# Kernel tuning notes

Measured on AMD Instinct MI355X. Metric: run time of the kernel, lower is better.

Reference implementation:

```python
import jax, jax.numpy as jnp
import numpy as np

B, N, D, H = 16, 729, 1152, 16
HD = D // H


def setup_inputs() -> dict:
    key = jax.random.key(0)
    ks = jax.random.split(key, 11)
    s = 0.02
    hidden_states = jax.random.normal(ks[0], (B, N, D), dtype=jnp.float32)
    # ToMe token sizes: positive merge counts in [1, 9)
    size = 1.0 + 8.0 * jax.random.uniform(ks[1], (B, N, 1), dtype=jnp.float32)
    Wq = s * jax.random.normal(ks[2], (D, D), dtype=jnp.float32)
    bq = jnp.zeros((D,), jnp.float32)
    Wk = s * jax.random.normal(ks[3], (D, D), dtype=jnp.float32)
    bk = jnp.zeros((D,), jnp.float32)
    Wv = s * jax.random.normal(ks[4], (D, D), dtype=jnp.float32)
    bv = jnp.zeros((D,), jnp.float32)
    Wo = s * jax.random.normal(ks[5], (D, D), dtype=jnp.float32)
    bo = jnp.zeros((D,), jnp.float32)
    return {"hidden_states": hidden_states, "size": size,
            "Wq": Wq, "bq": bq, "Wk": Wk, "bk": bk,
            "Wv": Wv, "bv": bv, "Wo": Wo, "bo": bo}


def reference(hidden_states, size, Wq, bq, Wk, bk, Wv, bv, Wo, bo):
    b, n, d = hidden_states.shape
    scale = HD ** -0.5
    # nn.Linear: y = x @ W.T + b
    def proj(W, bias):
        y = jnp.einsum('bnd,ed->bne', hidden_states, W) + bias
        return y.reshape(b, n, H, HD).transpose(0, 2, 1, 3)  # (B,H,N,HD)
    q = proj(Wq, bq)
    k = proj(Wk, bk)
    v = proj(Wv, bv)
    # additive log-size bias over keys: (B,1,1,N) broadcast to (B,H,N,N)
    size_bias_log = jnp.log(size[:, :, 0])[:, None, None, :]
    metric = k.mean(axis=1)  # mean over heads -> (B, N, HD)
    attn = jnp.einsum('bhqd,bhkd->bhqk', q, k) * scale + size_bias_log
    attn = jax.nn.softmax(attn.astype(jnp.float32), axis=-1).astype(q.dtype)
    out = jnp.einsum('bhqk,bhkd->bhqd', attn, v)  # (B,H,N,HD)
    out = out.transpose(0, 2, 1, 3).reshape(b, n, d)
    out = jnp.einsum('bnd,ed->bne', out, Wo) + bo
    return (out, attn, metric)
```

## Files before the change

### kernel.cpp

```cpp
#include <hip/hip_runtime.h>

#define BB    16
#define NN    729
#define DD    1152
#define HH_   16
#define HDIM  72
#define NPAD  736
#define HDPAD 96
#define MTOK  (BB*NN)
#define ESTR  768

typedef __attribute__((ext_vector_type(8))) short bf16x8;
typedef __attribute__((ext_vector_type(4))) float f32x4;

__device__ __forceinline__ unsigned short f2bf(float f) {
  unsigned u = __float_as_uint(f);
  u += 0x7fffu + ((u >> 16) & 1u);
  return (unsigned short)(u >> 16);
}
__device__ __forceinline__ float bf2f(unsigned short s) {
  return __uint_as_float(((unsigned)s) << 16);
}

__device__ __forceinline__ void gload_lds16(const void* g, void* l) {
  __builtin_amdgcn_global_load_lds(
      (const __attribute__((address_space(1))) void*)(unsigned long long)g,
      (__attribute__((address_space(3))) void*)(unsigned)(unsigned long long)l,
      16, 0, 0);
}

__global__ __launch_bounds__(256) void cast_x_kernel(const float* __restrict__ in,
                                                     unsigned short* __restrict__ out, int n4) {
  int i = blockIdx.x * 256 + threadIdx.x;
  for (; i < n4; i += gridDim.x * 256) {
    float4 v = ((const float4*)in)[i];
    uint2 o;
    o.x = (unsigned)f2bf(v.x) | ((unsigned)f2bf(v.y) << 16);
    o.y = (unsigned)f2bf(v.z) | ((unsigned)f2bf(v.w) << 16);
    ((uint2*)out)[i] = o;
  }
}

__global__ __launch_bounds__(256) void cast_w_kernel(const float* __restrict__ wq,
                                                     const float* __restrict__ wk,
                                                     const float* __restrict__ wv,
                                                     const float* __restrict__ wo,
                                                     unsigned short* __restrict__ out) {
  const int per = DD * DD / 4;
  int i = blockIdx.x * 256 + threadIdx.x;
  for (; i < 4 * per; i += gridDim.x * 256) {
    const int which = i / per, off = i - which * per;
    const float* src = which == 0 ? wq : which == 1 ? wk : which == 2 ? wv : wo;
    float4 v = ((const float4*)src)[off];
    uint2 o;
    o.x = (unsigned)f2bf(v.x) | ((unsigned)f2bf(v.y) << 16);
    o.y = (unsigned)f2bf(v.z) | ((unsigned)f2bf(v.w) << 16);
    ((uint2*)out)[i] = o;
  }
}

__global__ __launch_bounds__(256) void ls_kernel(const float* __restrict__ tsize,
                                                 float* __restrict__ LSg) {
  const int idx = blockIdx.x * 256 + threadIdx.x;
  if (idx < BB * NPAD) {
    const int b = idx / NPAD, k = idx - b * NPAD;
    LSg[idx] = (k < NN) ? __logf(tsize[b * NN + k]) : -1e30f;
  }
}

__global__ __launch_bounds__(256) void pad_kernel(unsigned short* __restrict__ Qb,
                                                  unsigned short* __restrict__ Kb) {
  const int bh = blockIdx.x, t = threadIdx.x;
  unsigned short* q = Qb + (size_t)bh * NPAD * HDPAD;
  unsigned short* k = Kb + (size_t)bh * NPAD * HDPAD;
  const uint4 z = {0, 0, 0, 0};
  for (int n = t; n < NPAD; n += 256) {
    uint4* qa = (uint4*)(q + n * HDPAD + 72);
    qa[0] = z; qa[1] = z; qa[2] = z;
    uint4* ka = (uint4*)(k + n * HDPAD + 72);
    ka[0] = z; ka[1] = z; ka[2] = z;
  }
  for (int i = t; i < 7 * 36; i += 256) {
    const int r = i / 36, c = i - (i / 36) * 36;
    ((unsigned*)(k + (size_t)(729 + r) * HDPAD))[c] = 0;
  }
}

__global__ __launch_bounds__(256) void vt_kernel(const unsigned short* __restrict__ Vtmp,
                                                 unsigned short* __restrict__ Vv) {
  __shared__ unsigned short tile[32][80];
  const int bh = blockIdx.x, kt = blockIdx.y;
  const int b = bh >> 4, hh = bh & 15;
  const int k0 = kt * 32;
  const int t = threadIdx.x;
  for (int i = t; i < 32 * 36; i += 256) {
    const int n = i / 36, c = i - (i / 36) * 36;
    unsigned u = 0;
    if (k0 + n < NN)
      u = *(const unsigned*)(Vtmp + ((size_t)(b * NN + k0 + n)) * DD + hh * HDIM + c * 2);
    tile[n][c * 2] = (unsigned short)(u & 0xffffu);
    tile[n][c * 2 + 1] = (unsigned short)(u >> 16);
  }
  for (int i = t; i < 32 * 8; i += 256) {
    const int n = i >> 3, c = i & 7;
    tile[n][72 + c] = 0;
  }
  __syncthreads();
  unsigned* dst = (unsigned*)(Vv + ((size_t)bh * 23 + kt) * 2560);
  for (int i2 = t; i2 < 1280; i2 += 256) {
    const int ni = i2 >> 8, rem = i2 & 255;
    const int lr = rem >> 4, np2 = (rem & 15) * 2;
    const int hd = ni * 16 + lr;
    const unsigned lo = tile[np2][hd], hi = tile[np2 + 1][hd];
    dst[i2] = lo | (hi << 16);
  }
}

#define PH_MID() \
  __builtin_amdgcn_s_barrier(); \
  asm volatile("s_waitcnt lgkmcnt(0)" ::: "memory"); \
  __builtin_amdgcn_sched_barrier(0); \
  __builtin_amdgcn_s_setprio(1)
#define PH_END() \
  __builtin_amdgcn_s_setprio(0); \
  __builtin_amdgcn_s_barrier()
#define QUAD(MB, NB) \
  _Pragma("unroll") for (int mr = 0; mr < 4; ++mr) \
  _Pragma("unroll") for (int nr = 0; nr < 2; ++nr) \
  _Pragma("unroll") for (int s = 0; s < 2; ++s) \
    acc[(MB) + mr][(NB) + nr] = __builtin_amdgcn_mfma_f32_16x16x32_bf16( \
        a[mr][s], b[(NB) + nr][s], acc[(MB) + mr][(NB) + nr], 0, 0, 0)

template <int MODE>
__global__ __launch_bounds__(512, 2) void gemm8_kernel(
    const unsigned short* __restrict__ A,
    const unsigned short* __restrict__ Bw,
    const float* __restrict__ bi0, const float* __restrict__ bi1, const float* __restrict__ bi2,
    unsigned short* __restrict__ O0, unsigned short* __restrict__ O1, unsigned short* __restrict__ O2,
    float* __restrict__ Of, int NBX, int nlim) {
  __shared__ __align__(16) char smem[131072];
  const int tid = threadIdx.x, w = tid >> 6, l = tid & 63;
  const int lr = l & 15, lh = l >> 4;
  const int wm = w >> 2, wn = w & 3;
  const int xr = (lr & 7) << 4;

  const int nblk = gridDim.x;
  const int xc = blockIdx.x & 7, oo = blockIdx.x >> 3;
  const int qq = nblk >> 3, rr = nblk & 7;
  const int wg = (xc < rr ? xc * (qq + 1) : rr * (qq + 1) + (xc - rr) * qq) + oo;
  const int m0 = (wg % NBX) * 256;
  const int n0 = (wg / NBX) * 256;

  f32x4 acc[8][4];
  const f32x4 fz = {0.f, 0.f, 0.f, 0.f};
#pragma unroll
  for (int i = 0; i < 8; ++i)
#pragma unroll
    for (int j = 0; j < 4; ++j) acc[i][j] = fz;

  auto stage = [&](const unsigned short* mat, int rlim, int row0, int kt, char* base) {
#pragma unroll
    for (int c = 0; c < 2; ++c) {
      const int beta = w * 1024 + c * 8192 + l * 16;
      const int g = beta ^ (((beta >> 7) & 7) << 4);
      int grow = row0 + (g >> 7);
      if (grow > rlim) grow = rlim;
      gload_lds16((const char*)mat + (size_t)grow * 2304 + kt * 128 + (g & 127), base + beta);
    }
  };
  bf16x8 a[4][2], b[4][2];
  auto lda = [&](char* Ab, int mh) {
#pragma unroll
    for (int mr = 0; mr < 4; ++mr)
#pragma unroll
      for (int s = 0; s < 2; ++s) {
        const int x = (wm * 128 + mh * 64 + mr * 16 + lr) * 128 + s * 64 + lh * 16;
        a[mr][s] = *(const bf16x8*)(Ab + (x ^ xr));
      }
  };
  auto ldb = [&](char* Bb, int nh) {
#pragma unroll
    for (int nr = 0; nr < 2; ++nr)
#pragma unroll
      for (int s = 0; s < 2; ++s) {
        const int x = (wn * 64 + nh * 32 + nr * 16 + lr) * 128 + s * 64 + lh * 16;
        b[nh * 2 + nr][s] = *(const bf16x8*)(Bb + (x ^ xr));
      }
  };

  stage(A, MTOK - 1, m0, 0, smem);
  stage(A, MTOK - 1, m0 + 128, 0, smem + 16384);
  stage(Bw, nlim, n0, 0, smem + 32768);
  stage(Bw, nlim, n0 + 128, 0, smem + 49152);
  stage(A, MTOK - 1, m0, 1, smem + 65536);
  stage(A, MTOK - 1, m0 + 128, 1, smem + 81920);
  asm volatile("s_waitcnt vmcnt(4)" ::: "memory");
  __builtin_amdgcn_s_barrier();

#pragma unroll 2
  for (int k = 0; k < 18; ++k) {
    char* Ac = smem + (k & 1) * 65536;
    char* Bc = Ac + 32768;
    char* An = smem + ((k + 1) & 1) * 65536;
    char* Bn = An + 32768;
    const int kb = (k + 1 < 18) ? k + 1 : 17;
    const int ka = (k + 2 < 18) ? k + 2 : 17;
    lda(Ac, 0);
    ldb(Bc, 0);
    stage(Bw, nlim, n0, kb, Bn);
    PH_MID();
    QUAD(0, 0);
    PH_END();
    ldb(Bc, 1);
    stage(Bw, nlim, n0 + 128, kb, Bn + 16384);
    PH_MID();
    QUAD(0, 2);
    PH_END();
    lda(Ac, 1);
    PH_MID();
    QUAD(4, 2);
    PH_END();
    stage(A, MTOK - 1, m0, ka, Ac);
    stage(A, MTOK - 1, m0 + 128, ka, Ac + 16384);
    PH_MID();
    QUAD(4, 0);
    __builtin_amdgcn_s_setprio(0);
    asm volatile("s_waitcnt vmcnt(4)" ::: "memory");
    __builtin_amdgcn_s_barrier();
  }

#pragma unroll
  for (int mi = 0; mi < 8; ++mi)
#pragma unroll
    for (int ni = 0; ni < 4; ++ni) {
      const int col = n0 + wn * 64 + ni * 16 + lr;
#pragma unroll
      for (int j = 0; j < 4; ++j) {
        const int row = m0 + wm * 128 + mi * 16 + lh * 4 + j;
        if (row < MTOK) {
          float v = acc[mi][ni][j];
          if (MODE == 0) {
            if (col < 3 * DD) {
              const int which = col / DD;
              const int ec = col - which * DD;
              const float* bias = which == 0 ? bi0 : (which == 1 ? bi1 : bi2);
              v += bias[ec];
              const unsigned short bv = f2bf(v);
              if (which == 2) {
                O2[(size_t)row * DD + ec] = bv;
              } else {
                const int h = ec / HDIM, hd = ec - h * HDIM;
                const int bb = row / NN, n = row - bb * NN;
                if (which == 0)
                  O0[(((size_t)bb * HH_ + h) * NPAD + n) * HDPAD + hd] = bv;
                else
                  O1[(((size_t)bb * HH_ + h) * NPAD + n) * HDPAD + hd] = bv;
              }
            }
          } else {
            if (col < DD)
              __builtin_nontemporal_store(v + bi0[col], Of + (size_t)row * DD + col);
          }
        }
      }
    }
}

__global__ __launch_bounds__(512, 4) void attn_kernel(
    const unsigned short* __restrict__ Qb,
    const unsigned short* __restrict__ Kb,
    const unsigned short* __restrict__ Vv,
    const float* __restrict__ LSg,
    float* __restrict__ attn_out,
    unsigned short* __restrict__ Ab) {
  __shared__ __align__(16) char smem[49280];
  unsigned short* Elds = (unsigned short*)smem;
  float* INV = (float*)(smem + 49152);
  float* red = (float*)smem;

  const int tid = threadIdx.x, w = tid >> 6, l = tid & 63;
  const int lr = l & 15, lh = l >> 4;

  const int id = blockIdx.x;
  const int nid = (id & 7) * 736 + (id >> 3);
  const int bh = nid / 23, qt = nid - bh * 23;
  const int b = bh >> 4, hh = bh & 15;
  const int q0 = qt * 32;

  const float scale = 0.11785113019775793f;
  const size_t kvbase = (size_t)bh * NPAD * HDPAD;
  const unsigned short* qp = Qb + kvbase + (size_t)q0 * HDPAD;

  bf16x8 aq[2][3];
#pragma unroll
  for (int mi = 0; mi < 2; ++mi)
#pragma unroll
    for (int ks = 0; ks < 3; ++ks)
      aq[mi][ks] = *(const bf16x8*)(qp + (size_t)(mi * 16 + lr) * HDPAD + ks * 32 + lh * 8);

  for (int kt = w; kt < 23; kt += 8) {
    const int k0 = kt * 32;
    const f32x4 fz = {0.f, 0.f, 0.f, 0.f};
    f32x4 acc[2][2];
    acc[0][0] = fz; acc[0][1] = fz; acc[1][0] = fz; acc[1][1] = fz;
    const unsigned short* kp = Kb + kvbase + (size_t)k0 * HDPAD;
#pragma unroll
    for (int ks = 0; ks < 3; ++ks) {
      const bf16x8 bk0 = *(const bf16x8*)(kp + (size_t)lr * HDPAD + ks * 32 + lh * 8);
      const bf16x8 bk1 = *(const bf16x8*)(kp + (size_t)(16 + lr) * HDPAD + ks * 32 + lh * 8);
#pragma unroll
      for (int mi = 0; mi < 2; ++mi) {
        acc[mi][0] = __builtin_amdgcn_mfma_f32_16x16x32_bf16(aq[mi][ks], bk0, acc[mi][0], 0, 0, 0);
        acc[mi][1] = __builtin_amdgcn_mfma_f32_16x16x32_bf16(aq[mi][ks], bk1, acc[mi][1], 0, 0, 0);
      }
    }
#pragma unroll
    for (int ni = 0; ni < 2; ++ni) {
      const int col = k0 + ni * 16 + lr;
      const float lsv = LSg[b * NPAD + col];
#pragma unroll
      for (int mi = 0; mi < 2; ++mi)
#pragma unroll
        for (int j = 0; j < 4; ++j) {
          const int row = mi * 16 + lh * 4 + j;
          const int swcol = col ^ ((row & 7) << 3);
          Elds[row * ESTR + swcol] = f2bf(__expf(acc[mi][ni][j] * scale + lsv));
        }
    }
  }
  __syncthreads();

  const int qv = NN - q0;
  {
    const int r = tid >> 4, sub = tid & 15;
    const unsigned short* er = Elds + r * ESTR;
    const int sw = (r & 7) << 3;
    uint2 ev[12];
    float s = 0.f;
#pragma unroll
    for (int i = 0; i < 12; ++i) {
      const int col = i * 64 + sub * 4;
      if (col < NPAD) {
        ev[i] = *(const uint2*)(er + (col ^ sw));
        s += bf2f(ev[i].x & 0xffffu) + bf2f(ev[i].x >> 16) +
             bf2f(ev[i].y & 0xffffu) + bf2f(ev[i].y >> 16);
      }
    }
#pragma unroll
    for (int o = 1; o < 16; o <<= 1) s += __shfl_xor(s, o);
    const float inv = 1.f / s;
    if (sub == 0) INV[r] = inv;
    if (r < qv) {
      float* ao = attn_out + ((size_t)bh * NN + (q0 + r)) * NN;
#pragma unroll
      for (int i = 0; i < 12; ++i) {
        const int col = i * 64 + sub * 4;
        if (col + 4 <= NN) {
          f32x4 o;
          o[0] = bf2f(ev[i].x & 0xffffu) * inv;
          o[1] = bf2f(ev[i].x >> 16) * inv;
          o[2] = bf2f(ev[i].y & 0xffffu) * inv;
          o[3] = bf2f(ev[i].y >> 16) * inv;
          __builtin_nontemporal_store(o, (f32x4*)(ao + col));
        } else if (col < NN) {
          __builtin_nontemporal_store(bf2f(ev[i].x & 0xffffu) * inv, ao + col);
        }
      }
    }
  }

  const int m = w & 1, kq = w >> 1;
  const f32x4 fz = {0.f, 0.f, 0.f, 0.f};
  f32x4 acc2[5];
#pragma unroll
  for (int ni = 0; ni < 5; ++ni) acc2[ni] = fz;
  {
    const int kt0 = kq * 6, kt1 = (kq == 3) ? 23 : kt0 + 6;
    const unsigned short* vbase = Vv + (size_t)bh * 58880 + (lr * 32 + lh * 8);
    const int row = m * 16 + lr;
    const int sw = (row & 7) << 3;
    const unsigned short* erow = Elds + row * ESTR;
    bf16x8 vA[5], vB[5];
#pragma unroll
    for (int ni = 0; ni < 5; ++ni) vA[ni] = *(const bf16x8*)(vbase + (kt0 * 5 + ni) * 512);
    for (int kt = kt0; kt < kt1; kt += 2) {
      const bool h1 = (kt + 1 < kt1);
      if (h1) {
#pragma unroll
        for (int ni = 0; ni < 5; ++ni) vB[ni] = *(const bf16x8*)(vbase + ((kt + 1) * 5 + ni) * 512);
      }
      {
        const int k0 = kt * 32;
        const bf16x8 ap = *(const bf16x8*)(erow + ((k0 + lh * 8) ^ sw));
#pragma unroll
        for (int ni = 0; ni < 5; ++ni)
          acc2[ni] = __builtin_amdgcn_mfma_f32_16x16x32_bf16(ap, vA[ni], acc2[ni], 0, 0, 0);
      }
      if (h1) {
        if (kt + 2 < kt1) {
#pragma unroll
          for (int ni = 0; ni < 5; ++ni) vA[ni] = *(const bf16x8*)(vbase + ((kt + 2) * 5 + ni) * 512);
        }
        const int k0 = (kt + 1) * 32;
        const bf16x8 ap = *(const bf16x8*)(erow + ((k0 + lh * 8) ^ sw));
#pragma unroll
        for (int ni = 0; ni < 5; ++ni)
          acc2[ni] = __builtin_amdgcn_mfma_f32_16x16x32_bf16(ap, vB[ni], acc2[ni], 0, 0, 0);
      }
    }
  }
  __syncthreads();

  if (kq > 0) {
    float* rd = red + ((kq - 1) * 2 + m) * 1344;
#pragma unroll
    for (int ni = 0; ni < 5; ++ni)
#pragma unroll
      for (int j = 0; j < 4; ++j)
        rd[(lh * 4 + j) * 84 + ni * 16 + lr] = acc2[ni][j];
  }
  __syncthreads();
  if (kq == 0) {
#pragma unroll
    for (int ni = 0; ni < 5; ++ni) {
      const int d = ni * 16 + lr;
      if (d < HDIM) {
#pragma unroll
        for (int j = 0; j < 4; ++j) {
          const int rrow = m * 16 + lh * 4 + j;
          const int q = q0 + rrow;
          if (q < NN) {
            const int ro = (lh * 4 + j) * 84 + ni * 16 + lr;
            const float s2 = acc2[ni][j] + red[m * 1344 + ro] + red[(2 + m) * 1344 + ro] +
                             red[(4 + m) * 1344 + ro];
            Ab[((size_t)b * NN + q) * DD + hh * HDIM + d] = f2bf(s2 * INV[rrow]);
          }
        }
      }
    }
  }
}

__global__ __launch_bounds__(256) void metric_kernel(const unsigned short* __restrict__ Kb,
                                                     float* __restrict__ out) {
  const int total = BB * NN * HDIM;
  int idx = blockIdx.x * 256 + threadIdx.x;
  for (; idx < total; idx += gridDim.x * 256) {
    const int b = idx / (NN * HDIM);
    const int rem = idx - b * NN * HDIM;
    const int n = rem / HDIM, d = rem - n * HDIM;
    const unsigned short* kp = Kb + (((size_t)b * HH_) * NPAD + n) * HDPAD + d;
    float s = 0.f;
#pragma unroll
    for (int h = 0; h < HH_; ++h) s += bf2f(kp[(size_t)h * NPAD * HDPAD]);
    __builtin_nontemporal_store(s * 0.0625f, out + idx);
  }
}

extern "C" void kernel_launch(void* const* d_in, const int* in_sizes, int n_in,
                              void* d_out, int out_size, void* d_ws, size_t ws_size,
                              hipStream_t stream) {
  const float* X = (const float*)d_in[0];
  const float* sz = (const float*)d_in[1];
  const float* Wq = (const float*)d_in[2];
  const float* bq = (const float*)d_in[3];
  const float* Wk = (const float*)d_in[4];
  const float* bk = (const float*)d_in[5];
  const float* Wv = (const float*)d_in[6];
  const float* bv = (const float*)d_in[7];
  const float* Wo = (const float*)d_in[8];
  const float* bo = (const float*)d_in[9];

  char* ws = (char*)d_ws;
  unsigned short* Xb = (unsigned short*)ws;
  unsigned short* Wb = (unsigned short*)(ws + 26873856);
  unsigned short* Qb = (unsigned short*)(ws + 37490688);
  unsigned short* Kb = (unsigned short*)(ws + 73666560);
  unsigned short* Vv = (unsigned short*)(ws + 109842432);
  unsigned short* Ab = (unsigned short*)(ws + 146018304);
  unsigned short* Vtmp = Ab;
  float* LSg = (float*)(ws + 172892160);

  float* out = (float*)d_out;
  float* attn = out + 13436928;
  float* metric = out + 149485824;

  ls_kernel<<<46, 256, 0, stream>>>(sz, LSg);
  cast_x_kernel<<<2048, 256, 0, stream>>>(X, Xb, 3359232);
  cast_w_kernel<<<2048, 256, 0, stream>>>(Wq, Wk, Wv, Wo, Wb);

  gemm8_kernel<0><<<644, 512, 0, stream>>>(Xb, Wb, bq, bk, bv, Qb, Kb, Vtmp, nullptr, 46, 3455);

  vt_kernel<<<dim3(256, 23), 256, 0, stream>>>(Vtmp, Vv);
  pad_kernel<<<256, 256, 0, stream>>>(Qb, Kb);
  metric_kernel<<<2048, 256, 0, stream>>>(Kb, metric);

  attn_kernel<<<5888, 512, 0, stream>>>(Qb, Kb, Vv, LSg, attn, Ab);

  gemm8_kernel<1><<<230, 512, 0, stream>>>(Ab, Wb + (size_t)3456 * 1152, bo, nullptr, nullptr,
                                           nullptr, nullptr, nullptr, out, 46, 1151);
}
```

Baseline: 497.9 us.

## Prefetch K tiles in registers and accumulate softmax row sums in fp32 during exp

The QK^T loop is unrolled into three fixed tile slots per wave, with K fragments double-buffered in registers so the next tile's loads overlap the current tile's MFMAs. Row sums of the exponentials are kept in fp32 registers during the exp pass, reduced across lanes with shuffles, and written to a small LDS array. This removes the separate LDS read-and-sum pass before normalisation. The change also alters numerics slightly: sums now come from unrounded fp32 values rather than bf16-rounded ones. It adds register pressure and about 1 KB more shared memory per block.

```diff
diff --git a/kernel.cpp b/kernel.cpp
--- a/kernel.cpp
+++ b/kernel.cpp
@@ -273,9 +273,10 @@
     const float* __restrict__ LSg,
     float* __restrict__ attn_out,
     unsigned short* __restrict__ Ab) {
-  __shared__ __align__(16) char smem[49280];
+  __shared__ __align__(16) char smem[50304];
   unsigned short* Elds = (unsigned short*)smem;
   float* INV = (float*)(smem + 49152);
+  float* rs = (float*)(smem + 49280);
   float* red = (float*)smem;
 
   const int tid = threadIdx.x, w = tid >> 6, l = tid & 63;
@@ -298,20 +299,31 @@
     for (int ks = 0; ks < 3; ++ks)
       aq[mi][ks] = *(const bf16x8*)(qp + (size_t)(mi * 16 + lr) * HDPAD + ks * 32 + lh * 8);
 
-  for (int kt = w; kt < 23; kt += 8) {
+  float pp[2][4];
+#pragma unroll
+  for (int mi = 0; mi < 2; ++mi)
+#pragma unroll
+    for (int j = 0; j < 4; ++j) pp[mi][j] = 0.f;
+
+  auto loadK = [&](int kt, bf16x8* dst) {
+    const unsigned short* kp = Kb + kvbase + (size_t)(kt * 32) * HDPAD;
+#pragma unroll
+    for (int ks = 0; ks < 3; ++ks) {
+      dst[ks * 2] = *(const bf16x8*)(kp + (size_t)lr * HDPAD + ks * 32 + lh * 8);
+      dst[ks * 2 + 1] = *(const bf16x8*)(kp + (size_t)(16 + lr) * HDPAD + ks * 32 + lh * 8);
+    }
+  };
+  auto process = [&](int kt, const bf16x8* kf) {
     const int k0 = kt * 32;
     const f32x4 fz = {0.f, 0.f, 0.f, 0.f};
     f32x4 acc[2][2];
     acc[0][0] = fz; acc[0][1] = fz; acc[1][0] = fz; acc[1][1] = fz;
-    const unsigned short* kp = Kb + kvbase + (size_t)k0 * HDPAD;
 #pragma unroll
     for (int ks = 0; ks < 3; ++ks) {
-      const bf16x8 bk0 = *(const bf16x8*)(kp + (size_t)lr * HDPAD + ks * 32 + lh * 8);
-      const bf16x8 bk1 = *(const bf16x8*)(kp + (size_t)(16 + lr) * HDPAD + ks * 32 + lh * 8);
 #pragma unroll
       for (int mi = 0; mi < 2; ++mi) {
-        acc[mi][0] = __builtin_amdgcn_mfma_f32_16x16x32_bf16(aq[mi][ks], bk0, acc[mi][0], 0, 0, 0);
-        acc[mi][1] = __builtin_amdgcn_mfma_f32_16x16x32_bf16(aq[mi][ks], bk1, acc[mi][1], 0, 0, 0);
+        acc[mi][0] = __builtin_amdgcn_mfma_f32_16x16x32_bf16(aq[mi][ks], kf[ks * 2], acc[mi][0], 0, 0, 0);
+        acc[mi][1] = __builtin_amdgcn_mfma_f32_16x16x32_bf16(aq[mi][ks], kf[ks * 2 + 1], acc[mi][1], 0, 0, 0);
       }
     }
 #pragma unroll
@@ -323,47 +335,63 @@
 #pragma unroll
         for (int j = 0; j < 4; ++j) {
           const int row = mi * 16 + lh * 4 + j;
-          const int swcol = col ^ ((row & 7) << 3);
-          Elds[row * ESTR + swcol] = f2bf(__expf(acc[mi][ni][j] * scale + lsv));
+          const float e = __expf(acc[mi][ni][j] * scale + lsv);
+          Elds[row * ESTR + (col ^ ((row & 7) << 3))] = f2bf(e);
+          pp[mi][j] += e;
         }
     }
+  };
+
+  {
+    const int myc = (w < 7) ? 3 : 2;
+    bf16x8 kfA[6], kfB[6];
+    loadK(w, kfA);
+    loadK(w + 8, kfB);
+    process(w, kfA);
+    if (myc > 2) loadK(w + 16, kfA);
+    process(w + 8, kfB);
+    if (myc > 2) process(w + 16, kfA);
+  }
+  {
+#pragma unroll
+    for (int mi = 0; mi < 2; ++mi)
+#pragma unroll
+      for (int j = 0; j < 4; ++j) {
+        float p = pp[mi][j];
+        p += __shfl_xor(p, 1);
+        p += __shfl_xor(p, 2);
+        p += __shfl_xor(p, 4);
+        p += __shfl_xor(p, 8);
+        if (lr == 0) rs[w * 32 + mi * 16 + lh * 4 + j] = p;
+      }
   }
   __syncthreads();
 
   const int qv = NN - q0;
   {
     const int r = tid >> 4, sub = tid & 15;
-    const unsigned short* er = Elds + r * ESTR;
-    const int sw = (r & 7) << 3;
-    uint2 ev[12];
-    float s = 0.f;
-#pragma unroll
-    for (int i = 0; i < 12; ++i) {
-      const int col = i * 64 + sub * 4;
-      if (col < NPAD) {
-        ev[i] = *(const uint2*)(er + (col ^ sw));
-        s += bf2f(ev[i].x & 0xffffu) + bf2f(ev[i].x >> 16) +
-             bf2f(ev[i].y & 0xffffu) + bf2f(ev[i].y >> 16);
-      }
-    }
-#pragma unroll
-    for (int o = 1; o < 16; o <<= 1) s += __shfl_xor(s, o);
+    float s = rs[r] + rs[32 + r] + rs[64 + r] + rs[96 + r] +
+              rs[128 + r] + rs[160 + r] + rs[192 + r] + rs[224 + r];
     const float inv = 1.f / s;
     if (sub == 0) INV[r] = inv;
     if (r < qv) {
+      const unsigned short* er = Elds + r * ESTR;
+      const int sw = (r & 7) << 3;
       float* ao = attn_out + ((size_t)bh * NN + (q0 + r)) * NN;
 #pragma unroll
       for (int i = 0; i < 12; ++i) {
         const int col = i * 64 + sub * 4;
         if (col + 4 <= NN) {
+          const uint2 ev = *(const uint2*)(er + (col ^ sw));
           f32x4 o;
-          o[0] = bf2f(ev[i].x & 0xffffu) * inv;
-          o[1] = bf2f(ev[i].x >> 16) * inv;
-          o[2] = bf2f(ev[i].y & 0xffffu) * inv;
-          o[3] = bf2f(ev[i].y >> 16) * inv;
+          o[0] = bf2f(ev.x & 0xffffu) * inv;
+          o[1] = bf2f(ev.x >> 16) * inv;
+          o[2] = bf2f(ev.y & 0xffffu) * inv;
+          o[3] = bf2f(ev.y >> 16) * inv;
           __builtin_nontemporal_store(o, (f32x4*)(ao + col));
         } else if (col < NN) {
-          __builtin_nontemporal_store(bf2f(ev[i].x & 0xffffu) * inv, ao + col);
+          const uint2 ev = *(const uint2*)(er + (col ^ sw));
+          __builtin_nontemporal_store(bf2f(ev.x & 0xffffu) * inv, ao + col);
         }
       }
     }
```

After: 519.8 us. +4.4%, slower.
